# Kernel optimization log

Measured on AMD Instinct MI355X. Metric: run time of the kernel, lower is better.

The kernel has to match this reference:

```python
import jax, jax.numpy as jnp
import numpy as np

N = 4096
IN_F = 512
OUT_F = 256
HEADS = 4
HEAD_DIM = OUT_F // HEADS


def setup_inputs() -> dict:
    key = jax.random.key(0)
    k_feat, k_adj, k_w, k_a = jax.random.split(key, 4)
    features = jax.random.normal(k_feat, (N, IN_F), dtype=jnp.float32)
    adj_matrix = jax.random.uniform(k_adj, (N, N), dtype=jnp.float32)
    # xavier-uniform-ish init scaled small
    W = jax.random.normal(k_w, (OUT_F, IN_F), dtype=jnp.float32) * (1.0 / np.sqrt(IN_F))
    a = jax.random.normal(k_a, (HEADS, 2 * HEAD_DIM), dtype=jnp.float32) * 0.1
    bias = jnp.zeros((OUT_F,), dtype=jnp.float32)
    return {"features": features, "adj_matrix": adj_matrix, "W": W, "a": a, "bias": bias}


def reference(features, adj_matrix, W, a, bias):
    n = features.shape[0]
    h = features @ W.T                      # [N, OUT_F]
    hh = h.reshape(n, HEADS, HEAD_DIM)      # [N, H, D]
    # e[i,j,h] = leaky_relu(<h_i, a[:, :D]> + <h_j, a[:, D:]>) -- additive decomposition
    e_src = jnp.einsum('nhd,hd->nh', hh, a[:, :HEAD_DIM])   # [N, H]
    e_dst = jnp.einsum('nhd,hd->nh', hh, a[:, HEAD_DIM:])   # [N, H]
    e = e_src[:, None, :] + e_dst[None, :, :]               # [N, N, H]
    e = jnp.where(e >= 0, e, 0.2 * e)                       # leaky_relu(0.2)
    mask = adj_matrix[:, :, None] > 0.1                     # [N, N, 1]
    e = jnp.where(mask, e, -jnp.inf)
    attention = jax.nn.softmax(e, axis=1)                   # softmax over j
    attention = jnp.nan_to_num(attention, nan=0.0)          # fully-masked rows -> 0
    attention_mean = attention.mean(axis=2)                 # [N, N]
    h_out = attention_mean @ h + bias                       # [N, OUT_F]
    return h_out
```

## Files before the change

### kernel.cpp

```cpp
#include <hip/hip_runtime.h>
#include <math.h>

#define NN      4096
#define INF_    512
#define OUTF    256
#define NHEAD   4
#define HDIM    64
#define KSPLIT  8

typedef __attribute__((ext_vector_type(8))) short  short8x;
typedef __attribute__((ext_vector_type(4))) float  float4x;
typedef __attribute__((ext_vector_type(2))) float  float2x;

__device__ __forceinline__ unsigned short f2bf(float x) {
    union { float f; unsigned int u; } c; c.f = x;
    unsigned int r = (c.u + 0x7FFFu + ((c.u >> 16) & 1u)) >> 16;
    return (unsigned short)r;
}
__device__ __forceinline__ unsigned int cvtpk_bf16(float lo, float hi) {
    unsigned int r;
    asm("v_cvt_pk_bf16_f32 %0, %1, %2" : "=v"(r) : "v"(lo), "v"(hi));
    return r;
}
__device__ __forceinline__ float2x bf2up(unsigned int u) {
    union { unsigned int x; float f; } lo, hi;
    lo.x = u << 16; hi.x = u & 0xFFFF0000u;
    float2x r; r[0] = lo.f; r[1] = hi.f; return r;
}
__device__ __forceinline__ float2x max2(float2x a, float2x b) {
    float2x r; r[0] = fmaxf(a[0], b[0]); r[1] = fmaxf(a[1], b[1]); return r;
}

__global__ __launch_bounds__(256) void k_hedge(const float* __restrict__ feat,
                                               const float* __restrict__ W,
                                               const float* __restrict__ a,
                                               const float* __restrict__ bias,
                                               const float* __restrict__ adj,
                                               unsigned short* __restrict__ hTf,
                                               float* __restrict__ es,
                                               unsigned short* __restrict__ Bt,
                                               unsigned short* __restrict__ Dt,
                                               unsigned short* __restrict__ mask,
                                               float* __restrict__ out) {
    __shared__ __align__(16) unsigned short lds_f[16 * 72];
    __shared__ __align__(16) unsigned short lds_w[256 * 72];
    const int tid  = threadIdx.x;

    if (blockIdx.x >= 256) {
        const int mb = blockIdx.x - 256;
        #pragma unroll
        for (int r = 0; r < 2; ++r) {
            const int row = mb * 2 + r;
            const float4x* arow4 = (const float4x*)(adj + (size_t)row * NN);
            unsigned int bits = 0;
            #pragma unroll
            for (int t = 0; t < 4; ++t) {
                float4x av = arow4[t * 256 + tid];
                #pragma unroll
                for (int e = 0; e < 4; ++e)
                    bits |= (av[e] > 0.1f ? 1u : 0u) << (t * 4 + e);
            }
            mask[(size_t)row * 256 + tid] = (unsigned short)bits;
        }
        return;
    }

    const int w    = tid >> 6;
    const int lane = tid & 63;
    const int lidx = lane & 15;
    const int quad = lane >> 4;
    const int i0   = blockIdx.x * 16;

    {
        float4x bv = *(const float4x*)(bias + ((tid * 4) & 255));
        float* ob = out + (size_t)i0 * OUTF;
        #pragma unroll
        for (int itr = 0; itr < 4; ++itr)
            *(float4x*)(ob + itr * 1024 + tid * 4) = bv;
    }

    const int fr = tid >> 4;
    const int fc = (tid & 15) * 4;
    const int wr = tid >> 2;
    const int wc = (tid & 3) * 16;

    float4x acc[4];
    #pragma unroll
    for (int q = 0; q < 4; ++q)
        acc[q] = (float4x){0.f, 0.f, 0.f, 0.f};

    for (int kt = 0; kt < INF_; kt += 64) {
        __syncthreads();
        {
            float4x v = *(const float4x*)&feat[(size_t)(i0 + fr) * INF_ + kt + fc];
            uint2 u;
            u.x = cvtpk_bf16(v[0], v[1]);
            u.y = cvtpk_bf16(v[2], v[3]);
            *(uint2*)&lds_f[fr * 72 + fc] = u;
        }
        #pragma unroll
        for (int p = 0; p < 4; ++p) {
            int row = p * 64 + wr;
            const float* src = &W[(size_t)row * INF_ + kt + wc];
            float4x v0 = *(const float4x*)(src);
            float4x v1 = *(const float4x*)(src + 4);
            float4x v2 = *(const float4x*)(src + 8);
            float4x v3 = *(const float4x*)(src + 12);
            union { short8x s; unsigned int u[4]; } p0, p1;
            p0.u[0] = cvtpk_bf16(v0[0], v0[1]); p0.u[1] = cvtpk_bf16(v0[2], v0[3]);
            p0.u[2] = cvtpk_bf16(v1[0], v1[1]); p0.u[3] = cvtpk_bf16(v1[2], v1[3]);
            p1.u[0] = cvtpk_bf16(v2[0], v2[1]); p1.u[1] = cvtpk_bf16(v2[2], v2[3]);
            p1.u[2] = cvtpk_bf16(v3[0], v3[1]); p1.u[3] = cvtpk_bf16(v3[2], v3[3]);
            *(short8x*)&lds_w[row * 72 + wc]     = p0.s;
            *(short8x*)&lds_w[row * 72 + wc + 8] = p1.s;
        }
        __syncthreads();
        #pragma unroll
        for (int kk = 0; kk < 2; ++kk) {
            short8x af = *(const short8x*)&lds_f[lidx * 72 + kk * 32 + quad * 8];
            short8x bw[4];
            #pragma unroll
            for (int nt = 0; nt < 4; ++nt)
                bw[nt] = *(const short8x*)&lds_w[(w * 64 + nt * 16 + lidx) * 72 + kk * 32 + quad * 8];
            #pragma unroll
            for (int nt = 0; nt < 4; ++nt)
                acc[nt] = __builtin_amdgcn_mfma_f32_16x16x32_bf16(af, bw[nt], acc[nt], 0, 0, 0);
        }
    }
    {
        const int ib    = i0 + quad * 4;
        const int kb2   = ib >> 5;
        const int quadB = (ib >> 3) & 3;
        const int e     = ib & 7;
        #pragma unroll
        for (int nt = 0; nt < 4; ++nt) {
            int n16 = w * 4 + nt;
            uint2 u;
            u.x = cvtpk_bf16(acc[nt][0], acc[nt][1]);
            u.y = cvtpk_bf16(acc[nt][2], acc[nt][3]);
            *(uint2*)&hTf[((size_t)(n16 * 128 + kb2) * 64 + quadB * 16 + lidx) * 8 + e] = u;
        }
    }
    float asrc[4], adst[4];
    #pragma unroll
    for (int nt = 0; nt < 4; ++nt) {
        asrc[nt] = a[w * 2 * HDIM + nt * 16 + lidx];
        adst[nt] = a[w * 2 * HDIM + HDIM + nt * 16 + lidx];
    }
    #pragma unroll
    for (int r = 0; r < 4; ++r) {
        float s = 0.f, d = 0.f;
        #pragma unroll
        for (int nt = 0; nt < 4; ++nt) {
            s += acc[nt][r] * asrc[nt];
            d += acc[nt][r] * adst[nt];
        }
        #pragma unroll
        for (int off = 1; off < 16; off <<= 1) {
            s += __shfl_xor(s, off);
            d += __shfl_xor(d, off);
        }
        if (lidx == 0) {
            int row = i0 + quad * 4 + r;
            es[row * NHEAD + w] = s;
            Bt[row * NHEAD + w] = f2bf(__expf(d));
            Dt[row * NHEAD + w] = f2bf(__expf(0.2f * d));
        }
    }
}

__global__ __launch_bounds__(256) void k_attn(const unsigned short* __restrict__ mask,
                                              const float* __restrict__ es,
                                              const unsigned short* __restrict__ Bt,
                                              const unsigned short* __restrict__ Dt,
                                              unsigned short* __restrict__ attn) {
    __shared__ float red[4][4];
    __shared__ float cfs[4];
    const int tid = threadIdx.x;
    const int wv  = tid >> 6;
    const int lane = tid & 63;
    const int i = blockIdx.x;

    const float4x esv = ((const float4x*)es)[i];
    float2x A01, A23, C01, C23;
    A01[0] = __expf(esv[0]); A01[1] = __expf(esv[1]);
    A23[0] = __expf(esv[2]); A23[1] = __expf(esv[3]);
    C01[0] = __expf(0.2f * esv[0]); C01[1] = __expf(0.2f * esv[1]);
    C23[0] = __expf(0.2f * esv[2]); C23[1] = __expf(0.2f * esv[3]);

    const unsigned int mbits = mask[(size_t)i * 256 + tid];
    const uint4* B4 = (const uint4*)Bt;
    const uint4* D4 = (const uint4*)Dt;

    float2x m01[4][4], m23[4][4];
    float2x den01 = (float2x){0.f, 0.f};
    float2x den23 = (float2x){0.f, 0.f};
    #pragma unroll
    for (int t = 0; t < 4; ++t) {
        int jv = t * 256 + tid;
        uint4 bu0 = B4[jv * 2], bu1 = B4[jv * 2 + 1];
        uint4 du0 = D4[jv * 2], du1 = D4[jv * 2 + 1];
        unsigned int bwv[8] = {bu0.x, bu0.y, bu0.z, bu0.w, bu1.x, bu1.y, bu1.z, bu1.w};
        unsigned int dwv[8] = {du0.x, du0.y, du0.z, du0.w, du1.x, du1.y, du1.z, du1.w};
        #pragma unroll
        for (int u = 0; u < 4; ++u) {
            float2x b01 = bf2up(bwv[u * 2]);
            float2x b23 = bf2up(bwv[u * 2 + 1]);
            float2x d01 = bf2up(dwv[u * 2]);
            float2x d23 = bf2up(dwv[u * 2 + 1]);
            float mf = (mbits & (1u << (t * 4 + u))) ? 1.f : 0.f;
            float2x mf2; mf2[0] = mf; mf2[1] = mf;
            m01[t][u] = mf2 * max2(A01 * b01, C01 * d01);
            m23[t][u] = mf2 * max2(A23 * b23, C23 * d23);
            den01 += m01[t][u];
            den23 += m23[t][u];
        }
    }
    float dh[4] = {den01[0], den01[1], den23[0], den23[1]};
    #pragma unroll
    for (int off = 1; off < 64; off <<= 1) {
        #pragma unroll
        for (int h = 0; h < 4; ++h)
            dh[h] += __shfl_xor(dh[h], off);
    }
    if (lane == 0) {
        #pragma unroll
        for (int h = 0; h < 4; ++h) red[wv][h] = dh[h];
    }
    __syncthreads();
    if (tid < 4)
        cfs[tid] = red[0][tid] + red[1][tid] + red[2][tid] + red[3][tid];
    __syncthreads();
    float sc[4];
    #pragma unroll
    for (int h = 0; h < 4; ++h) {
        float den = cfs[h];
        sc[h] = den > 0.f ? 0.25f / den : 0.f;
    }

    unsigned short* orow = attn + (size_t)i * NN;
    #pragma unroll
    for (int t = 0; t < 4; ++t) {
        int jv = t * 256 + tid;
        float pv[4];
        #pragma unroll
        for (int u = 0; u < 4; ++u) {
            pv[u] = sc[0] * m01[t][u][0] + sc[1] * m01[t][u][1]
                  + sc[2] * m23[t][u][0] + sc[3] * m23[t][u][1];
        }
        uint2 o;
        o.x = cvtpk_bf16(pv[0], pv[1]);
        o.y = cvtpk_bf16(pv[2], pv[3]);
        *(uint2*)&orow[jv * 4] = o;
    }
}

__global__ __launch_bounds__(256) void k_out_gemm(const unsigned short* __restrict__ attn,
                                                  const unsigned short* __restrict__ hTf,
                                                  float* __restrict__ out) {
    __shared__ __align__(16) unsigned short lds_a[2][32 * 72];
    const int tid  = threadIdx.x;
    const int w    = tid >> 6;
    const int lane = tid & 63;
    const int lidx = lane & 15;
    const int quad = lane >> 4;
    const int i0    = blockIdx.y * 32;
    const int kbase = blockIdx.x * (NN / KSPLIT);
    const int kbb   = kbase >> 5;
    const int sr   = tid >> 3;
    const int sc   = (tid & 7) * 8;

    float4x acc[2][4];
    #pragma unroll
    for (int p = 0; p < 2; ++p)
        #pragma unroll
        for (int q = 0; q < 4; ++q)
            acc[p][q] = (float4x){0.f, 0.f, 0.f, 0.f};

    const unsigned short* arow = &attn[(size_t)(i0 + sr) * NN + kbase + sc];

    short8x pa;
    pa = *(const short8x*)(arow);
    *(short8x*)&lds_a[0][sr * 72 + sc] = pa;
    pa = *(const short8x*)(arow + 64);
    __syncthreads();

    const int KSTEPS = (NN / KSPLIT) / 64;
    #pragma unroll
    for (int ks = 0; ks < KSTEPS; ++ks) {
        const int cur = ks & 1;
        if (ks + 1 < KSTEPS)
            *(short8x*)&lds_a[cur ^ 1][sr * 72 + sc] = pa;
        if (ks + 2 < KSTEPS)
            pa = *(const short8x*)(arow + (ks + 2) * 64);
        #pragma unroll
        for (int kk = 0; kk < 2; ++kk) {
            const int kb2 = kbb + ks * 2 + kk;
            short8x af[2], bfr[4];
            #pragma unroll
            for (int it = 0; it < 2; ++it)
                af[it]  = *(const short8x*)&lds_a[cur][(it * 16 + lidx) * 72 + kk * 32 + quad * 8];
            #pragma unroll
            for (int nt = 0; nt < 4; ++nt)
                bfr[nt] = *(const short8x*)&hTf[((size_t)((w * 4 + nt) * 128 + kb2) * 64 + lane) * 8];
            #pragma unroll
            for (int it = 0; it < 2; ++it)
                #pragma unroll
                for (int nt = 0; nt < 4; ++nt)
                    acc[it][nt] = __builtin_amdgcn_mfma_f32_16x16x32_bf16(
                        af[it], bfr[nt], acc[it][nt], 0, 0, 0);
        }
        __syncthreads();
    }
    #pragma unroll
    for (int it = 0; it < 2; ++it)
        #pragma unroll
        for (int nt = 0; nt < 4; ++nt)
            #pragma unroll
            for (int rr = 0; rr < 4; ++rr) {
                int row = i0 + it * 16 + quad * 4 + rr;
                int col = w * 64 + nt * 16 + lidx;
                unsafeAtomicAdd(&out[(size_t)row * OUTF + col], acc[it][nt][rr]);
            }
}

extern "C" void kernel_launch(void* const* d_in, const int* in_sizes, int n_in,
                              void* d_out, int out_size, void* d_ws, size_t ws_size,
                              hipStream_t stream) {
    const float* feat = (const float*)d_in[0];
    const float* adj  = (const float*)d_in[1];
    const float* W    = (const float*)d_in[2];
    const float* a    = (const float*)d_in[3];
    const float* bias = (const float*)d_in[4];
    float* out = (float*)d_out;

    char* ws = (char*)d_ws;
    float*          es    = (float*)(ws + 0);
    unsigned short* Btb   = (unsigned short*)(ws + (64u << 10));
    unsigned short* Dtb   = (unsigned short*)(ws + (96u << 10));
    unsigned short* mask  = (unsigned short*)(ws + (128u << 10));
    unsigned short* hTf   = (unsigned short*)(ws + (2560u << 10));
    unsigned short* attn  = (unsigned short*)(ws + (5120u << 10));

    k_hedge    <<<2304,              256, 0, stream>>>(feat, W, a, bias, adj, hTf, es, Btb, Dtb, mask, out);
    k_attn     <<<NN,                256, 0, stream>>>(mask, es, Btb, Dtb, attn);
    k_out_gemm <<<dim3(KSPLIT, 128), 256, 0, stream>>>(attn, hTf, out);
}
```

Baseline: 168.9 us.

## Process four attention rows per block, reusing loaded Bt/Dt column data

The attention kernel now handles four query rows per block instead of one, loading each column's bf16 exp factors once and reusing them across the four rows. To limit register pressure it no longer stores the masked products and instead recomputes them in the output pass. The goal is to cut redundant global loads of Bt/Dt and per-block overhead, at the cost of extra ALU work, more shuffles for the 16 reductions, and fewer blocks (1024).

Result: slower. 177.8 us (+5.2%).

```diff
diff --git a/kernel.cpp b/kernel.cpp
--- a/kernel.cpp
+++ b/kernel.cpp
@@ -174,84 +174,115 @@
                                               const unsigned short* __restrict__ Bt,
                                               const unsigned short* __restrict__ Dt,
                                               unsigned short* __restrict__ attn) {
-    __shared__ float red[4][4];
-    __shared__ float cfs[4];
+    __shared__ float red[4][16];
+    __shared__ float cfs[16];
     const int tid = threadIdx.x;
     const int wv  = tid >> 6;
     const int lane = tid & 63;
-    const int i = blockIdx.x;
-
-    const float4x esv = ((const float4x*)es)[i];
-    float2x A01, A23, C01, C23;
-    A01[0] = __expf(esv[0]); A01[1] = __expf(esv[1]);
-    A23[0] = __expf(esv[2]); A23[1] = __expf(esv[3]);
-    C01[0] = __expf(0.2f * esv[0]); C01[1] = __expf(0.2f * esv[1]);
-    C23[0] = __expf(0.2f * esv[2]); C23[1] = __expf(0.2f * esv[3]);
-
-    const unsigned int mbits = mask[(size_t)i * 256 + tid];
+    const int i0 = blockIdx.x * 4;
+
+    float2x Aa[4], Ab[4], Ca[4], Cb[4];
+    unsigned int mb[4];
+    #pragma unroll
+    for (int r = 0; r < 4; ++r) {
+        const float4x esv = ((const float4x*)es)[i0 + r];
+        Aa[r][0] = __expf(esv[0]); Aa[r][1] = __expf(esv[1]);
+        Ab[r][0] = __expf(esv[2]); Ab[r][1] = __expf(esv[3]);
+        Ca[r][0] = __expf(0.2f * esv[0]); Ca[r][1] = __expf(0.2f * esv[1]);
+        Cb[r][0] = __expf(0.2f * esv[2]); Cb[r][1] = __expf(0.2f * esv[3]);
+        mb[r] = mask[(size_t)(i0 + r) * 256 + tid];
+    }
+
     const uint4* B4 = (const uint4*)Bt;
     const uint4* D4 = (const uint4*)Dt;
 
-    float2x m01[4][4], m23[4][4];
-    float2x den01 = (float2x){0.f, 0.f};
-    float2x den23 = (float2x){0.f, 0.f};
+    unsigned int bw[4][8], dw[4][8];
     #pragma unroll
     for (int t = 0; t < 4; ++t) {
         int jv = t * 256 + tid;
         uint4 bu0 = B4[jv * 2], bu1 = B4[jv * 2 + 1];
         uint4 du0 = D4[jv * 2], du1 = D4[jv * 2 + 1];
-        unsigned int bwv[8] = {bu0.x, bu0.y, bu0.z, bu0.w, bu1.x, bu1.y, bu1.z, bu1.w};
-        unsigned int dwv[8] = {du0.x, du0.y, du0.z, du0.w, du1.x, du1.y, du1.z, du1.w};
+        bw[t][0] = bu0.x; bw[t][1] = bu0.y; bw[t][2] = bu0.z; bw[t][3] = bu0.w;
+        bw[t][4] = bu1.x; bw[t][5] = bu1.y; bw[t][6] = bu1.z; bw[t][7] = bu1.w;
+        dw[t][0] = du0.x; dw[t][1] = du0.y; dw[t][2] = du0.z; dw[t][3] = du0.w;
+        dw[t][4] = du1.x; dw[t][5] = du1.y; dw[t][6] = du1.z; dw[t][7] = du1.w;
+    }
+
+    float2x da[4], db[4];
+    #pragma unroll
+    for (int r = 0; r < 4; ++r) {
+        da[r] = (float2x){0.f, 0.f};
+        db[r] = (float2x){0.f, 0.f};
+    }
+    #pragma unroll
+    for (int t = 0; t < 4; ++t) {
         #pragma unroll
         for (int u = 0; u < 4; ++u) {
-            float2x b01 = bf2up(bwv[u * 2]);
-            float2x b23 = bf2up(bwv[u * 2 + 1]);
-            float2x d01 = bf2up(dwv[u * 2]);
-            float2x d23 = bf2up(dwv[u * 2 + 1]);
-            float mf = (mbits & (1u << (t * 4 + u))) ? 1.f : 0.f;
-            float2x mf2; mf2[0] = mf; mf2[1] = mf;
-            m01[t][u] = mf2 * max2(A01 * b01, C01 * d01);
-            m23[t][u] = mf2 * max2(A23 * b23, C23 * d23);
-            den01 += m01[t][u];
-            den23 += m23[t][u];
-        }
-    }
-    float dh[4] = {den01[0], den01[1], den23[0], den23[1]};
+            float2x b01 = bf2up(bw[t][u * 2]);
+            float2x b23 = bf2up(bw[t][u * 2 + 1]);
+            float2x q01 = bf2up(dw[t][u * 2]);
+            float2x q23 = bf2up(dw[t][u * 2 + 1]);
+            #pragma unroll
+            for (int r = 0; r < 4; ++r) {
+                float f = (mb[r] & (1u << (t * 4 + u))) ? 1.f : 0.f;
+                float2x fv; fv[0] = f; fv[1] = f;
+                da[r] += fv * max2(Aa[r] * b01, Ca[r] * q01);
+                db[r] += fv * max2(Ab[r] * b23, Cb[r] * q23);
+            }
+        }
+    }
+    float dh[16];
+    #pragma unroll
+    for (int r = 0; r < 4; ++r) {
+        dh[r * 4 + 0] = da[r][0]; dh[r * 4 + 1] = da[r][1];
+        dh[r * 4 + 2] = db[r][0]; dh[r * 4 + 3] = db[r][1];
+    }
     #pragma unroll
     for (int off = 1; off < 64; off <<= 1) {
         #pragma unroll
-        for (int h = 0; h < 4; ++h)
+        for (int h = 0; h < 16; ++h)
             dh[h] += __shfl_xor(dh[h], off);
     }
     if (lane == 0) {
         #pragma unroll
-        for (int h = 0; h < 4; ++h) red[wv][h] = dh[h];
+        for (int h = 0; h < 16; ++h) red[wv][h] = dh[h];
     }
     __syncthreads();
-    if (tid < 4)
+    if (tid < 16)
         cfs[tid] = red[0][tid] + red[1][tid] + red[2][tid] + red[3][tid];
     __syncthreads();
-    float sc[4];
-    #pragma unroll
-    for (int h = 0; h < 4; ++h) {
-        float den = cfs[h];
-        sc[h] = den > 0.f ? 0.25f / den : 0.f;
-    }
-
-    unsigned short* orow = attn + (size_t)i * NN;
+    float sc[4][4];
+    #pragma unroll
+    for (int r = 0; r < 4; ++r)
+        #pragma unroll
+        for (int h = 0; h < 4; ++h) {
+            float e0 = cfs[r * 4 + h];
+            sc[r][h] = e0 > 0.f ? 0.25f / e0 : 0.f;
+        }
+
     #pragma unroll
     for (int t = 0; t < 4; ++t) {
         int jv = t * 256 + tid;
-        float pv[4];
-        #pragma unroll
-        for (int u = 0; u < 4; ++u) {
-            pv[u] = sc[0] * m01[t][u][0] + sc[1] * m01[t][u][1]
-                  + sc[2] * m23[t][u][0] + sc[3] * m23[t][u][1];
-        }
-        uint2 o;
-        o.x = cvtpk_bf16(pv[0], pv[1]);
-        o.y = cvtpk_bf16(pv[2], pv[3]);
-        *(uint2*)&orow[jv * 4] = o;
+        #pragma unroll
+        for (int r = 0; r < 4; ++r) {
+            float pv[4];
+            #pragma unroll
+            for (int u = 0; u < 4; ++u) {
+                float2x b01 = bf2up(bw[t][u * 2]);
+                float2x b23 = bf2up(bw[t][u * 2 + 1]);
+                float2x q01 = bf2up(dw[t][u * 2]);
+                float2x q23 = bf2up(dw[t][u * 2 + 1]);
+                float2x ta = max2(Aa[r] * b01, Ca[r] * q01);
+                float2x tb = max2(Ab[r] * b23, Cb[r] * q23);
+                float s = sc[r][0] * ta[0] + sc[r][1] * ta[1]
+                        + sc[r][2] * tb[0] + sc[r][3] * tb[1];
+                pv[u] = (mb[r] & (1u << (t * 4 + u))) ? s : 0.f;
+            }
+            uint2 o;
+            o.x = cvtpk_bf16(pv[0], pv[1]);
+            o.y = cvtpk_bf16(pv[2], pv[3]);
+            *(uint2*)&attn[(size_t)(i0 + r) * NN + jv * 4] = o;
+        }
     }
 }
 
@@ -343,6 +374,6 @@
     unsigned short* attn  = (unsigned short*)(ws + (5120u << 10));
 
     k_hedge    <<<2304,              256, 0, stream>>>(feat, W, a, bias, adj, hTf, es, Btb, Dtb, mask, out);
-    k_attn     <<<NN,                256, 0, stream>>>(mask, es, Btb, Dtb, attn);
+    k_attn     <<<NN / 4,            256, 0, stream>>>(mask, es, Btb, Dtb, attn);
     k_out_gemm <<<dim3(KSPLIT, 128), 256, 0, stream>>>(attn, hTf, out);
 }
```
